# Kernel tuning notes

Hardware: AMD Instinct MI355X
Metric: run time of the kernel (lower is better)

Reference implementation:

```python
import jax, jax.numpy as jnp
import numpy as np

SIGMA = 0.1  # init kwarg sigma
B_CONST = 1.0  # init kwarg b
EPS = 1e-5


def setup_inputs() -> dict:
    key = jax.random.key(0)
    k1, k2 = jax.random.split(key)
    shape = (4, 256, 48, 48)  # N, C, H, W
    return {
        "featureT": jax.random.normal(k1, shape, dtype=jnp.float32),
        "featureI": jax.random.normal(k2, shape, dtype=jnp.float32),
    }


def reference(featureT, featureI):
    # center both features by the target's per-channel mean (over N, H, W)
    meanT = featureT.mean(axis=(0, 2, 3), keepdims=True)
    fI = featureI - meanT
    fT = featureT - meanT
    # l2-normalize channelwise (dim=1)
    fI = fI / jnp.linalg.norm(fI, axis=1, keepdims=True)
    fT = fT / jnp.linalg.norm(fT, axis=1, keepdims=True)
    N, C, H, W = fT.shape
    P = H * W
    # per-sample all-pairs patch cosine similarity: dist[n,p,h,w] = sum_c fT[n,c,p] * fI[n,c,h,w]
    # (equivalent to the per-sample F.conv2d with 1x1 filters from patch_decomposition)
    dist = jnp.einsum('ncp,nchw->nphw', fT.reshape(N, C, P), fI)  # [N, P, H, W]
    raw_dist = (1.0 - dist) / 2.0
    # relative distances along the patch axis (axis=1)
    div = jnp.min(raw_dist, axis=1, keepdims=True)
    relative_dist = raw_dist / (div + EPS)
    # contextual similarity: exp-weighted normalization along axis=1
    Wmat = jnp.exp((B_CONST - relative_dist) / SIGMA)
    CX = Wmat / jnp.sum(Wmat, axis=1, keepdims=True)
    # max over spatial dims (3 then 2), mean over patches
    CX = CX.max(axis=(2, 3))  # [N, P]
    CX = CX.mean(axis=1)      # [N]
    CX_B = -jnp.log(CX)       # [N]
    loss = jnp.mean(CX_B)
    return (loss, CX_B)
```

## Files before the change

### kernel.cpp

```cpp
#include <hip/hip_runtime.h>
#include <hip/hip_fp16.h>

#define NN 4
#define CC 256
#define PP 2304
#define EPSV 1e-5f

typedef __attribute__((ext_vector_type(8))) short bf16x8;
typedef __attribute__((ext_vector_type(4))) float f32x4;

struct alignas(8) h4 { __half2 a, b; };

__device__ inline unsigned fenc(float f) {
  unsigned b = __float_as_uint(f);
  return (b & 0x80000000u) ? ~b : (b | 0x80000000u);
}
__device__ inline float fdec(unsigned e) {
  unsigned b = (e & 0x80000000u) ? (e ^ 0x80000000u) : ~e;
  return __uint_as_float(b);
}

__device__ inline unsigned short f2bf(float x) {
  unsigned u = __float_as_uint(x);
  unsigned r = (u + 0x7FFFu + ((u >> 16) & 1u)) >> 16;
  return (unsigned short)r;
}

__device__ inline void gload_lds16(const unsigned short* g, unsigned short* l) {
  __builtin_amdgcn_global_load_lds(
      (const __attribute__((address_space(1))) void*)g,
      (__attribute__((address_space(3))) void*)l, 16, 0, 0);
}

__global__ __launch_bounds__(256) void k_init(unsigned* __restrict__ divu,
                                              float* __restrict__ S,
                                              float* __restrict__ meanT,
                                              float* __restrict__ cxsum) {
  int i = blockIdx.x * 256 + threadIdx.x;
  divu[i] = 0xFFFFFFFFu;
  S[i] = 0.f;
  if (i < CC) meanT[i] = 0.f;
  if (i < 4) cxsum[i] = 0.f;
}

__global__ __launch_bounds__(256) void k_mean(const float* __restrict__ fT,
                                              float* __restrict__ meanT) {
  int c = blockIdx.x, n = blockIdx.y, t = threadIdx.x;
  const float* base = fT + ((size_t)n * CC + c) * PP;
  float s = 0.f;
  for (int p = t; p < PP; p += 256) s += base[p];
  for (int o = 32; o > 0; o >>= 1) s += __shfl_down(s, o);
  __shared__ float red[4];
  if ((t & 63) == 0) red[t >> 6] = s;
  __syncthreads();
  if (t == 0) atomicAdd(&meanT[c], red[0] + red[1] + red[2] + red[3]);
}

__global__ __launch_bounds__(256) void k_norm(const float* __restrict__ fT,
                                              const float* __restrict__ fI,
                                              const float* __restrict__ meanT,
                                              unsigned short* __restrict__ A,
                                              unsigned short* __restrict__ B) {
  int n = blockIdx.y;
  int p0 = blockIdx.x * 16;
  int t = threadIdx.x;
  int tc = t >> 4, tp = t & 15;
  __shared__ float cT[16][257];
  __shared__ float cI[16][257];
  __shared__ float redT[16][17], redI[16][17];
  __shared__ float inv[2][16];
  float aT = 0.f, aI = 0.f;
  int p = p0 + tp;
  for (int c0 = 0; c0 < CC; c0 += 16) {
    int c = c0 + tc;
    float m = meanT[c] * (1.0f / (float)(NN * PP));
    size_t g = (size_t)n * CC * PP + (size_t)c * PP + p;
    float vT = fT[g] - m;
    float vI = fI[g] - m;
    cT[tp][c] = vT; cI[tp][c] = vI;
    aT += vT * vT; aI += vI * vI;
  }
  redT[tp][tc] = aT; redI[tp][tc] = aI;
  __syncthreads();
  if (t < 16) {
    float sT = 0.f, sI = 0.f;
    for (int k = 0; k < 16; k++) { sT += redT[t][k]; sI += redI[t][k]; }
    inv[0][t] = 1.0f / sqrtf(sT);
    inv[1][t] = 1.0f / sqrtf(sI);
  }
  __syncthreads();
#pragma unroll
  for (int it = 0; it < 2; it++) {
    int task = it * 256 + t;
    int ps = task >> 5;
    int ch = task & 31;
    float iA = inv[0][ps], iB = inv[1][ps];
    unsigned short va[8], vb[8];
#pragma unroll
    for (int e = 0; e < 8; e++) {
      va[e] = f2bf(cT[ps][ch * 8 + e] * iA);
      vb[e] = f2bf(cI[ps][ch * 8 + e] * iB);
    }
    size_t o = ((size_t)(n * PP + p0 + ps)) * CC + ch * 8;
    *(int4*)(A + o) = *(const int4*)va;
    *(int4*)(B + o) = *(const int4*)vb;
  }
}

__global__ __launch_bounds__(256) void k_gemm(const unsigned short* __restrict__ A,
                                              const unsigned short* __restrict__ B,
                                              __half* __restrict__ raw,
                                              unsigned* __restrict__ divu) {
  int n  = blockIdx.z;
  int i0 = blockIdx.y * 128;
  int j0 = blockIdx.x * 128;
  int t  = threadIdx.x;
  int lane = t & 63;
  int w = t >> 6;
  int wi = w >> 1, wj = w & 1;
  int lr = lane & 15, lq = lane >> 4;

  __shared__ __align__(16) char smem[34816];
  unsigned short* As = (unsigned short*)smem;
  unsigned short* Bs = (unsigned short*)(smem + 16384);
  __half* r16 = (__half*)smem;
  __shared__ unsigned cmin[128];
  if (t < 128) cmin[t] = 0xFFFFFFFFu;

  f32x4 acc[4][4];
#pragma unroll
  for (int a = 0; a < 4; a++)
#pragma unroll
    for (int b = 0; b < 4; b++) acc[a][b] = (f32x4){0.f, 0.f, 0.f, 0.f};

  const size_t baseA = ((size_t)(n * PP + i0)) * CC;
  const size_t baseB = ((size_t)(n * PP + j0)) * CC;
  int lrow8 = lane >> 3;
  int lseg  = (lane & 7) ^ (lrow8 & 7);

  for (int k0 = 0; k0 < CC; k0 += 64) {
    if (k0) __syncthreads();
#pragma unroll
    for (int it = 0; it < 4; it++) {
      int sb = (w * 4 + it) * 64;
      int row = (w * 4 + it) * 8 + lrow8;
      gload_lds16(A + baseA + (size_t)row * CC + k0 + lseg * 8, As + sb * 8);
      gload_lds16(B + baseB + (size_t)row * CC + k0 + lseg * 8, Bs + sb * 8);
    }
    __syncthreads();
#pragma unroll
    for (int ks = 0; ks < 2; ks++) {
      bf16x8 af[4], bf[4];
#pragma unroll
      for (int ti = 0; ti < 4; ti++) {
        int row = wi * 64 + ti * 16 + lr;
        int slot = row * 8 + ((ks * 4 + lq) ^ (lr & 7));
        af[ti] = *(const bf16x8*)&As[slot * 8];
      }
#pragma unroll
      for (int tj = 0; tj < 4; tj++) {
        int row = wj * 64 + tj * 16 + lr;
        int slot = row * 8 + ((ks * 4 + lq) ^ (lr & 7));
        bf[tj] = *(const bf16x8*)&Bs[slot * 8];
      }
#pragma unroll
      for (int ti = 0; ti < 4; ti++)
#pragma unroll
        for (int tj = 0; tj < 4; tj++)
          acc[ti][tj] = __builtin_amdgcn_mfma_f32_16x16x32_bf16(af[ti], bf[tj], acc[ti][tj], 0, 0, 0);
    }
  }

  __syncthreads();
#pragma unroll
  for (int tj = 0; tj < 4; tj++) {
    float mx = -1e30f;
    int cj = wj * 64 + tj * 16 + lr;
#pragma unroll
    for (int ti = 0; ti < 4; ti++) {
#pragma unroll
      for (int r = 0; r < 4; r++) {
        float g = acc[ti][tj][r];
        mx = fmaxf(mx, g);
        int ci = wi * 64 + ti * 16 + lq * 4 + r;
        r16[ci * 136 + cj] = __float2half((1.0f - g) * 0.5f);
      }
    }
    atomicMin(&cmin[cj], fenc((1.0f - mx) * 0.5f));
  }
  __syncthreads();
#pragma unroll
  for (int m = 0; m < 8; m++) {
    int chunk = m * 256 + t;
    int row = chunk >> 4, cs = chunk & 15;
    int4 v = *(const int4*)&r16[row * 136 + cs * 8];
    *(int4*)(raw + ((size_t)(n * PP + i0 + row)) * PP + j0 + cs * 8) = v;
  }
  if (t < 128) atomicMin(&divu[n * PP + j0 + t], cmin[t]);
}

__global__ __launch_bounds__(256) void k_colsum(const __half* __restrict__ raw,
                                                const unsigned* __restrict__ divu,
                                                float* __restrict__ S) {
  int n = blockIdx.y;
  int j0 = blockIdx.x * 256;
  int rz = blockIdx.z;
  int t = threadIdx.x;
  int lane = t & 63, w = t >> 6;
  int j = j0 + lane * 4;

  uint4 dv = *(const uint4*)(divu + n * PP + j);
  float4 sc;
  sc.x = -10.0f / (fdec(dv.x) + EPSV);
  sc.y = -10.0f / (fdec(dv.y) + EPSV);
  sc.z = -10.0f / (fdec(dv.z) + EPSV);
  sc.w = -10.0f / (fdec(dv.w) + EPSV);

  const __half* base = raw + (size_t)n * PP * PP;
  float4 s = {0.f, 0.f, 0.f, 0.f};
  int i0 = rz * 96;
  for (int i = i0 + w; i < i0 + 96; i += 4) {
    h4 hv = *(const h4*)(base + (size_t)i * PP + j);
    float2 f01 = __half22float2(hv.a);
    float2 f23 = __half22float2(hv.b);
    s.x += __expf(f01.x * sc.x);
    s.y += __expf(f01.y * sc.y);
    s.z += __expf(f23.x * sc.z);
    s.w += __expf(f23.y * sc.w);
  }
  __shared__ float4 red4[4][64];
  red4[w][lane] = s;
  __syncthreads();
  if (t < 64) {
    float4 a = red4[0][t], b = red4[1][t], c = red4[2][t], d = red4[3][t];
    int jj = j0 + t * 4;
    atomicAdd(&S[n * PP + jj + 0], a.x + b.x + c.x + d.x);
    atomicAdd(&S[n * PP + jj + 1], a.y + b.y + c.y + d.y);
    atomicAdd(&S[n * PP + jj + 2], a.z + b.z + c.z + d.z);
    atomicAdd(&S[n * PP + jj + 3], a.w + b.w + c.w + d.w);
  }
}

__global__ __launch_bounds__(256) void k_logscale(const unsigned* __restrict__ divu,
                                                  const float* __restrict__ S,
                                                  float* __restrict__ scale,
                                                  float* __restrict__ lnS) {
  int i = blockIdx.x * 256 + threadIdx.x;
  float d = fdec(divu[i]);
  scale[i] = -10.0f / (d + EPSV);
  lnS[i] = logf(S[i]);
}

__global__ __launch_bounds__(256) void k_rowmax(const __half* __restrict__ raw,
                                                const float* __restrict__ scale,
                                                const float* __restrict__ lnS,
                                                float* __restrict__ cxsum) {
  int t = threadIdx.x, lane = t & 63, w = t >> 6;
  int r = blockIdx.x * 4 + w;
  int n = r / PP;
  const __half* rp = raw + (size_t)r * PP;
  const float* scp = scale + n * PP;
  const float* lnp = lnS + n * PP;
  float m = -1e30f;
#pragma unroll
  for (int c = 0; c < 9; c++) {
    int j = c * 256 + lane * 4;
    h4 hv = *(const h4*)(rp + j);
    float4 sc = *(const float4*)(scp + j);
    float4 ls = *(const float4*)(lnp + j);
    float2 f01 = __half22float2(hv.a);
    float2 f23 = __half22float2(hv.b);
    m = fmaxf(m, fmaf(f01.x, sc.x, -ls.x));
    m = fmaxf(m, fmaf(f01.y, sc.y, -ls.y));
    m = fmaxf(m, fmaf(f23.x, sc.z, -ls.z));
    m = fmaxf(m, fmaf(f23.y, sc.w, -ls.w));
  }
  for (int o = 32; o > 0; o >>= 1) m = fmaxf(m, __shfl_down(m, o));
  __shared__ float red[4];
  if (lane == 0) red[w] = __expf(m);
  __syncthreads();
  if (t == 0)
    atomicAdd(&cxsum[n], (red[0] + red[1] + red[2] + red[3]) * (1.0f / (float)PP));
}

__global__ void k_final(const float* __restrict__ cxsum, float* __restrict__ out) {
  int t = threadIdx.x;
  float cxb = 0.f;
  if (t < 4) {
    cxb = -logf(cxsum[t]);
    out[1 + t] = cxb;
  }
  for (int o = 2; o > 0; o >>= 1) cxb += __shfl_down(cxb, o);
  if (t == 0) out[0] = cxb * 0.25f;
}

extern "C" void kernel_launch(void* const* d_in, const int* in_sizes, int n_in,
                              void* d_out, int out_size, void* d_ws, size_t ws_size,
                              hipStream_t stream) {
  const float* fT = (const float*)d_in[0];
  const float* fI = (const float*)d_in[1];
  float* out = (float*)d_out;

  char* w = (char*)d_ws;
  float* meanT   = (float*)w;
  unsigned* divu = (unsigned*)(w + 1024);
  float* S       = (float*)(w + 1024 + 36864);
  float* scale   = (float*)(w + 1024 + 2 * 36864);
  float* lnS     = (float*)(w + 1024 + 3 * 36864);
  float* cxsum   = (float*)(w + 1024 + 4 * 36864);
  size_t off = 1024 + 4 * 36864 + 1024;
  unsigned short* A = (unsigned short*)(w + off);
  unsigned short* B = (unsigned short*)(w + off + 4718592);
  __half* raw = (__half*)(w + off + 2 * 4718592);

  k_init<<<36, 256, 0, stream>>>(divu, S, meanT, cxsum);
  k_mean<<<dim3(CC, NN), 256, 0, stream>>>(fT, meanT);
  k_norm<<<dim3(PP / 16, NN), 256, 0, stream>>>(fT, fI, meanT, A, B);
  k_gemm<<<dim3(PP / 128, PP / 128, NN), 256, 0, stream>>>(A, B, raw, divu);
  k_colsum<<<dim3(PP / 256, NN, 24), 256, 0, stream>>>(raw, divu, S);
  k_logscale<<<36, 256, 0, stream>>>(divu, S, scale, lnS);
  k_rowmax<<<dim3(PP * NN / 4), 256, 0, stream>>>(raw, scale, lnS, cxsum);
  k_final<<<1, 64, 0, stream>>>(cxsum, out);
}
```

Measured before the change: 153.0 us.

## Store similarity matrix transposed and swap column/row reduction strategies

The GEMM epilogue now writes the half-precision distance matrix transposed, so each patch-axis column becomes a contiguous row. The column-sum kernel can then use one wavefront per row with no atomics, and the row-max becomes a strided column reduction using atomicMax on encoded floats, followed by a new k_cx kernel. The init kernel is folded into k_mean, which now loops over the batch and writes the finished mean directly instead of using atomicAdd. This trades atomics in the exp-sum pass for atomics in the cheaper max pass, and adds one extra small launch.

After: 131.0 us. 1.17x faster.

```diff
diff --git a/kernel.cpp b/kernel.cpp
--- a/kernel.cpp
+++ b/kernel.cpp
@@ -32,28 +32,28 @@
       (__attribute__((address_space(3))) void*)l, 16, 0, 0);
 }
 
-__global__ __launch_bounds__(256) void k_init(unsigned* __restrict__ divu,
-                                              float* __restrict__ S,
+__global__ __launch_bounds__(256) void k_mean(const float* __restrict__ fT,
                                               float* __restrict__ meanT,
+                                              unsigned* __restrict__ divu,
+                                              unsigned* __restrict__ M,
                                               float* __restrict__ cxsum) {
-  int i = blockIdx.x * 256 + threadIdx.x;
-  divu[i] = 0xFFFFFFFFu;
-  S[i] = 0.f;
-  if (i < CC) meanT[i] = 0.f;
-  if (i < 4) cxsum[i] = 0.f;
-}
-
-__global__ __launch_bounds__(256) void k_mean(const float* __restrict__ fT,
-                                              float* __restrict__ meanT) {
-  int c = blockIdx.x, n = blockIdx.y, t = threadIdx.x;
-  const float* base = fT + ((size_t)n * CC + c) * PP;
+  int c = blockIdx.x, t = threadIdx.x;
   float s = 0.f;
-  for (int p = t; p < PP; p += 256) s += base[p];
+  for (int n = 0; n < NN; n++) {
+    const float* base = fT + (size_t)n * CC * PP + (size_t)c * PP;
+    for (int p = t; p < PP; p += 256) s += base[p];
+  }
   for (int o = 32; o > 0; o >>= 1) s += __shfl_down(s, o);
   __shared__ float red[4];
   if ((t & 63) == 0) red[t >> 6] = s;
   __syncthreads();
-  if (t == 0) atomicAdd(&meanT[c], red[0] + red[1] + red[2] + red[3]);
+  if (t == 0) meanT[c] = (red[0] + red[1] + red[2] + red[3]) / (float)(NN * PP);
+  if (t < 36) {
+    int idx = c * 36 + t;
+    divu[idx] = 0xFFFFFFFFu;
+    M[idx] = 0u;
+  }
+  if (blockIdx.x == 0 && t < 4) cxsum[t] = 0.f;
 }
 
 __global__ __launch_bounds__(256) void k_norm(const float* __restrict__ fT,
@@ -73,7 +73,7 @@
   int p = p0 + tp;
   for (int c0 = 0; c0 < CC; c0 += 16) {
     int c = c0 + tc;
-    float m = meanT[c] * (1.0f / (float)(NN * PP));
+    float m = meanT[c];
     size_t g = (size_t)n * CC * PP + (size_t)c * PP + p;
     float vT = fT[g] - m;
     float vI = fI[g] - m;
@@ -109,7 +109,7 @@
 
 __global__ __launch_bounds__(256) void k_gemm(const unsigned short* __restrict__ A,
                                               const unsigned short* __restrict__ B,
-                                              __half* __restrict__ raw,
+                                              __half* __restrict__ rawt,
                                               unsigned* __restrict__ divu) {
   int n  = blockIdx.z;
   int i0 = blockIdx.y * 128;
@@ -120,10 +120,10 @@
   int wi = w >> 1, wj = w & 1;
   int lr = lane & 15, lq = lane >> 4;
 
-  __shared__ __align__(16) char smem[34816];
+  __shared__ __align__(16) char smem[33792];
   unsigned short* As = (unsigned short*)smem;
   unsigned short* Bs = (unsigned short*)(smem + 16384);
-  __half* r16 = (__half*)smem;
+  __half* r16t = (__half*)smem;
   __shared__ unsigned cmin[128];
   if (t < 128) cmin[t] = 0xFFFFFFFFu;
 
@@ -178,13 +178,15 @@
     int cj = wj * 64 + tj * 16 + lr;
 #pragma unroll
     for (int ti = 0; ti < 4; ti++) {
+      alignas(8) unsigned short pk[4];
 #pragma unroll
       for (int r = 0; r < 4; r++) {
         float g = acc[ti][tj][r];
         mx = fmaxf(mx, g);
-        int ci = wi * 64 + ti * 16 + lq * 4 + r;
-        r16[ci * 136 + cj] = __float2half((1.0f - g) * 0.5f);
+        pk[r] = __half_as_ushort(__float2half((1.0f - g) * 0.5f));
       }
+      int ci = wi * 64 + ti * 16 + lq * 4;
+      *(short4*)&r16t[cj * 132 + ci] = *(const short4*)pk;
     }
     atomicMin(&cmin[cj], fenc((1.0f - mx) * 0.5f));
   }
@@ -193,52 +195,32 @@
   for (int m = 0; m < 8; m++) {
     int chunk = m * 256 + t;
     int row = chunk >> 4, cs = chunk & 15;
-    int4 v = *(const int4*)&r16[row * 136 + cs * 8];
-    *(int4*)(raw + ((size_t)(n * PP + i0 + row)) * PP + j0 + cs * 8) = v;
+    int2 lo = *(const int2*)&r16t[row * 132 + cs * 8];
+    int2 hi = *(const int2*)&r16t[row * 132 + cs * 8 + 4];
+    int4 v = {lo.x, lo.y, hi.x, hi.y};
+    *(int4*)(rawt + ((size_t)(n * PP + j0 + row)) * PP + i0 + cs * 8) = v;
   }
   if (t < 128) atomicMin(&divu[n * PP + j0 + t], cmin[t]);
 }
 
-__global__ __launch_bounds__(256) void k_colsum(const __half* __restrict__ raw,
+__global__ __launch_bounds__(256) void k_colsum(const __half* __restrict__ rawt,
                                                 const unsigned* __restrict__ divu,
                                                 float* __restrict__ S) {
-  int n = blockIdx.y;
-  int j0 = blockIdx.x * 256;
-  int rz = blockIdx.z;
-  int t = threadIdx.x;
-  int lane = t & 63, w = t >> 6;
-  int j = j0 + lane * 4;
-
-  uint4 dv = *(const uint4*)(divu + n * PP + j);
-  float4 sc;
-  sc.x = -10.0f / (fdec(dv.x) + EPSV);
-  sc.y = -10.0f / (fdec(dv.y) + EPSV);
-  sc.z = -10.0f / (fdec(dv.z) + EPSV);
-  sc.w = -10.0f / (fdec(dv.w) + EPSV);
-
-  const __half* base = raw + (size_t)n * PP * PP;
-  float4 s = {0.f, 0.f, 0.f, 0.f};
-  int i0 = rz * 96;
-  for (int i = i0 + w; i < i0 + 96; i += 4) {
-    h4 hv = *(const h4*)(base + (size_t)i * PP + j);
+  int t = threadIdx.x, lane = t & 63, w = t >> 6;
+  int r = blockIdx.x * 4 + w;
+  float d = fdec(divu[r]);
+  float sc = -10.0f / (d + EPSV);
+  const __half* rp = rawt + (size_t)r * PP;
+  float s = 0.f;
+#pragma unroll
+  for (int c = 0; c < 9; c++) {
+    h4 hv = *(const h4*)(rp + c * 256 + lane * 4);
     float2 f01 = __half22float2(hv.a);
     float2 f23 = __half22float2(hv.b);
-    s.x += __expf(f01.x * sc.x);
-    s.y += __expf(f01.y * sc.y);
-    s.z += __expf(f23.x * sc.z);
-    s.w += __expf(f23.y * sc.w);
-  }
-  __shared__ float4 red4[4][64];
-  red4[w][lane] = s;
-  __syncthreads();
-  if (t < 64) {
-    float4 a = red4[0][t], b = red4[1][t], c = red4[2][t], d = red4[3][t];
-    int jj = j0 + t * 4;
-    atomicAdd(&S[n * PP + jj + 0], a.x + b.x + c.x + d.x);
-    atomicAdd(&S[n * PP + jj + 1], a.y + b.y + c.y + d.y);
-    atomicAdd(&S[n * PP + jj + 2], a.z + b.z + c.z + d.z);
-    atomicAdd(&S[n * PP + jj + 3], a.w + b.w + c.w + d.w);
-  }
+    s += __expf(f01.x * sc) + __expf(f01.y * sc) + __expf(f23.x * sc) + __expf(f23.y * sc);
+  }
+  for (int o = 32; o > 0; o >>= 1) s += __shfl_down(s, o);
+  if (lane == 0) S[r] = s;
 }
 
 __global__ __launch_bounds__(256) void k_logscale(const unsigned* __restrict__ divu,
@@ -251,36 +233,54 @@
   lnS[i] = logf(S[i]);
 }
 
-__global__ __launch_bounds__(256) void k_rowmax(const __half* __restrict__ raw,
+__global__ __launch_bounds__(256) void k_rowmax(const __half* __restrict__ rawt,
                                                 const float* __restrict__ scale,
                                                 const float* __restrict__ lnS,
-                                                float* __restrict__ cxsum) {
-  int t = threadIdx.x, lane = t & 63, w = t >> 6;
-  int r = blockIdx.x * 4 + w;
-  int n = r / PP;
-  const __half* rp = raw + (size_t)r * PP;
-  const float* scp = scale + n * PP;
-  const float* lnp = lnS + n * PP;
-  float m = -1e30f;
-#pragma unroll
-  for (int c = 0; c < 9; c++) {
-    int j = c * 256 + lane * 4;
-    h4 hv = *(const h4*)(rp + j);
-    float4 sc = *(const float4*)(scp + j);
-    float4 ls = *(const float4*)(lnp + j);
+                                                unsigned* __restrict__ M) {
+  int n = blockIdx.y;
+  int i0 = blockIdx.x * 256;
+  int rz = blockIdx.z;
+  int t = threadIdx.x;
+  int lane = t & 63, w = t >> 6;
+  int i = i0 + lane * 4;
+
+  float4 m = {-1e30f, -1e30f, -1e30f, -1e30f};
+  int j0 = rz * 96;
+  for (int j = j0 + w; j < j0 + 96; j += 4) {
+    float scj = scale[n * PP + j];
+    float lsj = lnS[n * PP + j];
+    h4 hv = *(const h4*)(rawt + ((size_t)(n * PP + j)) * PP + i);
     float2 f01 = __half22float2(hv.a);
     float2 f23 = __half22float2(hv.b);
-    m = fmaxf(m, fmaf(f01.x, sc.x, -ls.x));
-    m = fmaxf(m, fmaf(f01.y, sc.y, -ls.y));
-    m = fmaxf(m, fmaf(f23.x, sc.z, -ls.z));
-    m = fmaxf(m, fmaf(f23.y, sc.w, -ls.w));
-  }
-  for (int o = 32; o > 0; o >>= 1) m = fmaxf(m, __shfl_down(m, o));
+    m.x = fmaxf(m.x, fmaf(f01.x, scj, -lsj));
+    m.y = fmaxf(m.y, fmaf(f01.y, scj, -lsj));
+    m.z = fmaxf(m.z, fmaf(f23.x, scj, -lsj));
+    m.w = fmaxf(m.w, fmaf(f23.y, scj, -lsj));
+  }
+  __shared__ float4 red4[4][64];
+  red4[w][lane] = m;
+  __syncthreads();
+  if (t < 64) {
+    float4 a = red4[0][t], b = red4[1][t], c = red4[2][t], d = red4[3][t];
+    int ii = i0 + t * 4;
+    atomicMax(&M[n * PP + ii + 0], fenc(fmaxf(fmaxf(a.x, b.x), fmaxf(c.x, d.x))));
+    atomicMax(&M[n * PP + ii + 1], fenc(fmaxf(fmaxf(a.y, b.y), fmaxf(c.y, d.y))));
+    atomicMax(&M[n * PP + ii + 2], fenc(fmaxf(fmaxf(a.z, b.z), fmaxf(c.z, d.z))));
+    atomicMax(&M[n * PP + ii + 3], fenc(fmaxf(fmaxf(a.w, b.w), fmaxf(c.w, d.w))));
+  }
+}
+
+__global__ __launch_bounds__(256) void k_cx(const unsigned* __restrict__ M,
+                                            float* __restrict__ cxsum) {
+  int b = blockIdx.x, t = threadIdx.x;
+  int idx = b * 256 + t;
+  int n = idx / PP;
+  float v = __expf(fdec(M[idx])) * (1.0f / (float)PP);
+  for (int o = 32; o > 0; o >>= 1) v += __shfl_down(v, o);
   __shared__ float red[4];
-  if (lane == 0) red[w] = __expf(m);
-  __syncthreads();
-  if (t == 0)
-    atomicAdd(&cxsum[n], (red[0] + red[1] + red[2] + red[3]) * (1.0f / (float)PP));
+  if ((t & 63) == 0) red[t >> 6] = v;
+  __syncthreads();
+  if (t == 0) atomicAdd(&cxsum[n], red[0] + red[1] + red[2] + red[3]);
 }
 
 __global__ void k_final(const float* __restrict__ cxsum, float* __restrict__ out) {
@@ -307,18 +307,19 @@
   float* S       = (float*)(w + 1024 + 36864);
   float* scale   = (float*)(w + 1024 + 2 * 36864);
   float* lnS     = (float*)(w + 1024 + 3 * 36864);
-  float* cxsum   = (float*)(w + 1024 + 4 * 36864);
-  size_t off = 1024 + 4 * 36864 + 1024;
+  unsigned* M    = (unsigned*)(w + 1024 + 4 * 36864);
+  float* cxsum   = (float*)(w + 1024 + 5 * 36864);
+  size_t off = 1024 + 5 * 36864 + 1024;
   unsigned short* A = (unsigned short*)(w + off);
   unsigned short* B = (unsigned short*)(w + off + 4718592);
-  __half* raw = (__half*)(w + off + 2 * 4718592);
-
-  k_init<<<36, 256, 0, stream>>>(divu, S, meanT, cxsum);
-  k_mean<<<dim3(CC, NN), 256, 0, stream>>>(fT, meanT);
+  __half* rawt = (__half*)(w + off + 2 * 4718592);
+
+  k_mean<<<256, 256, 0, stream>>>(fT, meanT, divu, M, cxsum);
   k_norm<<<dim3(PP / 16, NN), 256, 0, stream>>>(fT, fI, meanT, A, B);
-  k_gemm<<<dim3(PP / 128, PP / 128, NN), 256, 0, stream>>>(A, B, raw, divu);
-  k_colsum<<<dim3(PP / 256, NN, 24), 256, 0, stream>>>(raw, divu, S);
+  k_gemm<<<dim3(PP / 128, PP / 128, NN), 256, 0, stream>>>(A, B, rawt, divu);
+  k_colsum<<<dim3(PP * NN / 4), 256, 0, stream>>>(rawt, divu, S);
   k_logscale<<<36, 256, 0, stream>>>(divu, S, scale, lnS);
-  k_rowmax<<<dim3(PP * NN / 4), 256, 0, stream>>>(raw, scale, lnS, cxsum);
+  k_rowmax<<<dim3(PP / 256, NN, 24), 256, 0, stream>>>(rawt, scale, lnS, M);
+  k_cx<<<36, 256, 0, stream>>>(M, cxsum);
   k_final<<<1, 64, 0, stream>>>(cxsum, out);
 }
```
